# Kernel optimization log

Hardware: AMD Instinct MI355X
Metric: run time of the kernel (lower is better)

Reference implementation:

```python
import jax, jax.numpy as jnp
import numpy as np

B, S, H, M, E = 64, 512, 1024, 26, 676  # batch, seq, hidden, max_nodes, max_edges (M*M)


def setup_inputs() -> dict:
    key = jax.random.key(0)
    ks = jax.random.split(key, 16)
    seq = jax.random.normal(ks[0], (B, S, H), jnp.float32)
    # ragged, strictly-increasing sentence-end offsets in [1, S-1], zero-padded tail
    rng = np.random.RandomState(0)
    off = np.zeros((B, M - 1), np.int64)
    for b in range(B):
        c = rng.randint(5, M)  # count of valid offsets per sample (ragged)
        off[b, :c] = np.sort(rng.choice(np.arange(1, S), size=c, replace=False))
    s = 1.0 / np.sqrt(H)
    s3 = 1.0 / np.sqrt(3 * H)
    return {
        'sequence_outputs': seq,
        'proof_offsets': jnp.asarray(off),
        'node_labels': jax.random.randint(ks[1], (B, M), 0, 2),
        'edge_labels': jax.random.randint(ks[2], (B, E), 0, 2),
        'W_naf': jax.random.normal(ks[3], (H, H), jnp.float32) * s,
        'b_naf': jnp.zeros((H,), jnp.float32),
        'W_cd': jax.random.normal(ks[4], (H, H), jnp.float32) * s,
        'b_cd': jnp.zeros((H,), jnp.float32),
        'W_co': jax.random.normal(ks[5], (H, 2), jnp.float32) * s,
        'b_co': jnp.zeros((2,), jnp.float32),
        'W_nd': jax.random.normal(ks[6], (H, H), jnp.float32) * s,
        'b_nd': jnp.zeros((H,), jnp.float32),
        'W_no': jax.random.normal(ks[7], (H, 2), jnp.float32) * s,
        'b_no': jnp.zeros((2,), jnp.float32),
        'W_ed': jax.random.normal(ks[8], (3 * H, H), jnp.float32) * s3,
        'b_ed': jnp.zeros((H,), jnp.float32),
        'W_eo': jax.random.normal(ks[9], (H, 2), jnp.float32) * s,
        'b_eo': jnp.zeros((2,), jnp.float32),
    }


def reference(sequence_outputs, proof_offsets, node_labels, edge_labels,
              W_naf, b_naf, W_cd, b_cd, W_co, b_co,
              W_nd, b_nd, W_no, b_no, W_ed, b_ed, W_eo, b_eo):
    Bx, Sx, Hx = sequence_outputs.shape
    Mx = node_labels.shape[1]
    Ex = edge_labels.shape[1]

    cls = sequence_outputs[:, 0, :]                       # [B,H]
    naf = cls @ W_naf + b_naf                             # NAF node embedding
    logits = jnp.tanh(cls @ W_cd + b_cd) @ W_co + b_co    # RobertaClassificationHead (eval: dropout=id)

    # segment-mean pooling via inclusive prefix sums: segment j = tokens (prev_j, off_j]
    P = jnp.cumsum(sequence_outputs, axis=1)              # [B,S,H]
    off = proof_offsets                                   # [B,M-1]
    prev = jnp.concatenate([jnp.zeros((Bx, 1), off.dtype), off[:, :-1]], axis=1)
    valid = off > 0                                       # [B,M-1]
    seg_sum = (jnp.take_along_axis(P, off[..., None], axis=1)
               - jnp.take_along_axis(P, prev[..., None], axis=1))  # [B,M-1,H]
    seg_len = jnp.maximum(off - prev, 1).astype(sequence_outputs.dtype)
    seg_mean = seg_sum / seg_len[..., None] * valid[..., None]

    count = valid.sum(axis=1)                             # nodes per sample (excl. NAF)
    # node embeddings: seg means at 0..count-1, NAF at index count, zeros after
    node_full = jnp.concatenate([seg_mean, jnp.zeros((Bx, 1, Hx), seg_mean.dtype)], axis=1)  # [B,M,H]
    idx = jnp.arange(Mx)
    node_full = node_full + (idx[None, :, None] == count[:, None, None]) * naf[:, None, :]

    # all-pairs edge features over n=count+1 nodes, row-major flat k=i*n+j, zero-padded to E
    n = count + 1                                         # [B]
    k = jnp.arange(Ex)                                    # [E]
    i = jnp.clip(k[None, :] // n[:, None], 0, Mx - 1)     # [B,E]
    j = jnp.clip(k[None, :] % n[:, None], 0, Mx - 1)
    valid_e = (k[None, :] < (n * n)[:, None])[..., None]
    ni = jnp.take_along_axis(node_full, i[..., None], axis=1)  # [B,E,H]
    nj = jnp.take_along_axis(node_full, j[..., None], axis=1)
    edge = jnp.concatenate([nj, ni, nj - ni], axis=-1) * valid_e  # [B,E,3H]

    node_logits = jnp.tanh(node_full @ W_nd + b_nd) @ W_no + b_no
    edge_logits = jnp.tanh(edge @ W_ed + b_ed) @ W_eo + b_eo
    return (logits, node_logits, edge_logits)
```

## Files before the change

### kernel.cpp

```cpp
#include <hip/hip_runtime.h>
#include <hip/hip_bf16.h>

#define B_ 64
#define S_ 512
#define H_ 1024
#define M_ 26
#define E_ 676

typedef short bf16x8 __attribute__((ext_vector_type(8)));
typedef float f32x4 __attribute__((ext_vector_type(4)));

__device__ __forceinline__ void gload16(const void* g, void* l) {
    __builtin_amdgcn_global_load_lds((const __attribute__((address_space(1))) unsigned int*)g,
                                     (__attribute__((address_space(3))) unsigned int*)l,
                                     16, 0, 0);
}

__device__ __forceinline__ float tanh_fast(float x) {
    float e = __expf(2.0f * x);
    return 1.0f - 2.0f * __builtin_amdgcn_rcpf(e + 1.0f);
}

__global__ __launch_bounds__(256) void k_stage1(
    const float* __restrict__ seq, const int* __restrict__ off,
    const float* __restrict__ Wnaf, const float* __restrict__ Wcd,
    const float* __restrict__ Wnd, const float* __restrict__ Wed,
    const float* __restrict__ bed, const float* __restrict__ Weo,
    const float* __restrict__ beo,
    __hip_bfloat16* __restrict__ Wt, int* __restrict__ count,
    float* __restrict__ econ, float* __restrict__ naf, float* __restrict__ cdh,
    float* __restrict__ node_sum) {
    __shared__ float smem[2048];
    int bid = blockIdx.x;
    int tid = threadIdx.x;

    if (bid < 1024) {
        int chunk = bid & 15, b = bid >> 4;
        int* offs = (int*)smem;
        int* cs = (int*)smem + 28;
        if (tid < M_ - 1) offs[tid] = off[b * (M_ - 1) + tid];
        __syncthreads();
        if (tid == 0) {
            int c = 0;
            while (c < M_ - 1 && offs[c] > 0) c++;
            cs[0] = c; cs[1] = (c > 0) ? offs[c - 1] : 0;
        }
        __syncthreads();
        int c = cs[0], offmax = cs[1];
        int t0 = chunk * 32;
        int ts = max(t0, 1), te = min(t0 + 31, offmax);
        if (ts > te) return;
        int m = 0;
        while (m < c && offs[m] < ts) m++;
        const float4* sq = (const float4*)(seq + (size_t)b * S_ * H_) + tid;
        int t = ts;
        while (t <= te) {
            int segEnd = min(offs[m], te);
            int L = segEnd - t + 1;
            const float4* p = sq + (size_t)t * (H_ / 4);
            float4 a0 = make_float4(0, 0, 0, 0);
            float4 a1 = a0, a2 = a0, a3 = a0;
            int u = 0;
            for (; u + 4 <= L; u += 4) {
                float4 v0 = p[(size_t)(u + 0) * (H_ / 4)];
                float4 v1 = p[(size_t)(u + 1) * (H_ / 4)];
                float4 v2 = p[(size_t)(u + 2) * (H_ / 4)];
                float4 v3 = p[(size_t)(u + 3) * (H_ / 4)];
                a0.x += v0.x; a0.y += v0.y; a0.z += v0.z; a0.w += v0.w;
                a1.x += v1.x; a1.y += v1.y; a1.z += v1.z; a1.w += v1.w;
                a2.x += v2.x; a2.y += v2.y; a2.z += v2.z; a2.w += v2.w;
                a3.x += v3.x; a3.y += v3.y; a3.z += v3.z; a3.w += v3.w;
            }
            for (; u < L; ++u) {
                float4 v0 = p[(size_t)u * (H_ / 4)];
                a0.x += v0.x; a0.y += v0.y; a0.z += v0.z; a0.w += v0.w;
            }
            a0.x += a1.x + a2.x + a3.x;
            a0.y += a1.y + a2.y + a3.y;
            a0.z += a1.z + a2.z + a3.z;
            a0.w += a1.w + a2.w + a3.w;
            float* dst = node_sum + ((size_t)(b * M_ + m)) * H_ + tid * 4;
            atomicAdd(dst + 0, a0.x); atomicAdd(dst + 1, a0.y);
            atomicAdd(dst + 2, a0.z); atomicAdd(dst + 3, a0.w);
            t = segEnd + 1;
            m++;
        }
    } else if (bid < 4096) {
        float (*T)[33] = (float(*)[33])smem;
        int e = bid - 1024;
        int s = e >> 10, rem = e & 1023;
        int bx = rem & 31, by = rem >> 5;
        int c = tid & 31, r0 = tid >> 5;
        const int HH = H_ * H_;
#pragma unroll
        for (int i = 0; i < 4; ++i) {
            int r = r0 + 8 * i;
            size_t k = by * 32 + r, n = bx * 32 + c;
            float v;
            if (s == 0)      v = Wnd[k * H_ + n];
            else if (s == 1) v = Wed[k * H_ + n] + Wed[2 * HH + k * H_ + n];
            else             v = Wed[HH + k * H_ + n] - Wed[2 * HH + k * H_ + n];
            T[r][c] = v;
        }
        __syncthreads();
#pragma unroll
        for (int i = 0; i < 4; ++i) {
            int rr = r0 + 8 * i;
            Wt[(size_t)(s * H_ + bx * 32 + rr) * H_ + by * 32 + c] = __float2bfloat16(T[c][rr]);
        }
    } else if (bid == 4096) {
        if (tid < 64) {
            int b = tid;
            int c = 0;
            for (int m = 0; m < M_ - 1; ++m) c += (off[b * (M_ - 1) + m] > 0) ? 1 : 0;
            count[b] = c;
        }
    } else if (bid == 4097) {
        float* s0 = smem; float* s1 = smem + 256;
        float a0 = 0.f, a1 = 0.f;
        for (int h = tid; h < H_; h += 256) {
            float t = tanh_fast(bed[h]);
            a0 += t * Weo[h * 2 + 0];
            a1 += t * Weo[h * 2 + 1];
        }
        s0[tid] = a0; s1[tid] = a1; __syncthreads();
        for (int o = 128; o > 0; o >>= 1) {
            if (tid < o) { s0[tid] += s0[tid + o]; s1[tid] += s1[tid + o]; }
            __syncthreads();
        }
        if (tid == 0) { econ[0] = s0[0] + beo[0]; econ[1] = s1[0] + beo[1]; }
    } else {
        float (*As)[64] = (float(*)[64])smem;
        float (*Bs)[64] = (float(*)[64])(smem + 1024);
        int e = bid - 4098;
        int bx = e & 31;
        int kbase = (e >> 5) * 128;
        const float* W;
        float* dst;
        int cbase;
        if (bx < 16) { W = Wnaf; dst = naf; cbase = bx * 64; }
        else         { W = Wcd;  dst = cdh; cbase = (bx - 16) * 64; }
        int tx = tid % 16, ty = tid / 16;
        float c[4][4] = {};
        int la_row = tid / 4;
        int la_k4  = (tid % 4) * 4;
        int lb_k   = tid / 16;
        int lb_c4  = (tid % 16) * 4;
        for (int k0 = 0; k0 < 128; k0 += 16) {
            float4 a = *(const float4*)(seq + (size_t)la_row * S_ * H_ + kbase + k0 + la_k4);
            *(float4*)(&Bs[lb_k][lb_c4]) =
                *(const float4*)(W + (size_t)(kbase + k0 + lb_k) * H_ + cbase + lb_c4);
            As[la_k4 + 0][la_row] = a.x;
            As[la_k4 + 1][la_row] = a.y;
            As[la_k4 + 2][la_row] = a.z;
            As[la_k4 + 3][la_row] = a.w;
            __syncthreads();
#pragma unroll
            for (int kk = 0; kk < 16; ++kk) {
                float4 av = *(const float4*)(&As[kk][ty * 4]);
                float4 bv = *(const float4*)(&Bs[kk][tx * 4]);
                c[0][0] += av.x * bv.x; c[0][1] += av.x * bv.y; c[0][2] += av.x * bv.z; c[0][3] += av.x * bv.w;
                c[1][0] += av.y * bv.x; c[1][1] += av.y * bv.y; c[1][2] += av.y * bv.z; c[1][3] += av.y * bv.w;
                c[2][0] += av.z * bv.x; c[2][1] += av.z * bv.y; c[2][2] += av.z * bv.z; c[2][3] += av.z * bv.w;
                c[3][0] += av.w * bv.x; c[3][1] += av.w * bv.y; c[3][2] += av.w * bv.z; c[3][3] += av.w * bv.w;
            }
            __syncthreads();
        }
#pragma unroll
        for (int i = 0; i < 4; ++i)
#pragma unroll
            for (int j = 0; j < 4; ++j)
                atomicAdd(dst + (size_t)(ty * 4 + i) * H_ + cbase + tx * 4 + j, c[i][j]);
    }
}

__global__ __launch_bounds__(256) void k_stage2(
    const float* __restrict__ sums, const int* __restrict__ off,
    const int* __restrict__ count, const float* __restrict__ naf,
    const float* __restrict__ bnaf, __hip_bfloat16* __restrict__ nodeB,
    const float* __restrict__ cdh, const float* __restrict__ bcd,
    const float* __restrict__ Wco, const float* __restrict__ bco,
    float* __restrict__ out) {
    __shared__ float smem[512];
    int bid = blockIdx.x;
    int tid = threadIdx.x;
    if (bid < 1664) {
        int b = bid / 26, m = bid - b * 26;
        int cnt = count[b];
        float4 v = make_float4(0, 0, 0, 0);
        const float4* row = (const float4*)(sums + ((size_t)(b * M_ + m)) * H_);
        if (m < M_ - 1) {
            int o = off[b * (M_ - 1) + m];
            if (o > 0) {
                int prev = (m > 0) ? off[b * (M_ - 1) + m - 1] : 0;
                float inv = 1.0f / (float)max(o - prev, 1);
                float4 s = row[tid];
                v = make_float4(s.x * inv, s.y * inv, s.z * inv, s.w * inv);
            }
        }
        if (m == cnt) {
            float4 a = ((const float4*)(naf + (size_t)b * H_))[tid];
            float4 bb = ((const float4*)bnaf)[tid];
            v.x += a.x + bb.x; v.y += a.y + bb.y; v.z += a.z + bb.z; v.w += a.w + bb.w;
        }
        __hip_bfloat16 __attribute__((aligned(8))) h[4] = {
            __float2bfloat16(v.x), __float2bfloat16(v.y),
            __float2bfloat16(v.z), __float2bfloat16(v.w)};
        *(ushort4*)(nodeB + ((size_t)(b * M_ + m)) * H_ + tid * 4) = *(const ushort4*)h;
    } else {
        int b = bid - 1664;
        float* s0 = smem; float* s1 = smem + 256;
        float a0 = 0.f, a1 = 0.f;
        for (int h = tid; h < H_; h += 256) {
            float t = tanh_fast(cdh[(size_t)b * H_ + h] + bcd[h]);
            a0 += t * Wco[h * 2 + 0];
            a1 += t * Wco[h * 2 + 1];
        }
        s0[tid] = a0; s1[tid] = a1; __syncthreads();
        for (int o = 128; o > 0; o >>= 1) {
            if (tid < o) { s0[tid] += s0[tid + o]; s1[tid] += s1[tid + o]; }
            __syncthreads();
        }
        if (tid == 0) { out[b * 2 + 0] = s0[0] + bco[0]; out[b * 2 + 1] = s1[0] + bco[1]; }
    }
}

#define GM 1664
#define GN 3072
#define GK 1024
__global__ __launch_bounds__(256) void k_mfma(const __hip_bfloat16* __restrict__ A,
                                              const __hip_bfloat16* __restrict__ Bt,
                                              float* __restrict__ C) {
    __shared__ __hip_bfloat16 As[128 * 32];
    __shared__ __hip_bfloat16 Bs[128 * 32];
    int tid = threadIdx.x;
    int wid = tid >> 6, ln = tid & 63;
    int row0 = blockIdx.y * 128, col0 = blockIdx.x * 128;
    const __hip_bfloat16* ga = A + (size_t)(row0 + wid * 16 + (ln >> 2)) * GK + (ln & 3) * 8;
    const __hip_bfloat16* gb = Bt + (size_t)(col0 + wid * 16 + (ln >> 2)) * GK + (ln & 3) * 8;
    __hip_bfloat16* lA = As + wid * 512;
    __hip_bfloat16* lB = Bs + wid * 512;
    int mrow = (wid >> 1) * 64, ncol = (wid & 1) * 64;
    int l15 = ln & 15, l4 = ln >> 4;
    f32x4 acc[4][4] = {};
    const __hip_bfloat16* pa = As + (size_t)(mrow + l15) * 32 + l4 * 8;
    const __hip_bfloat16* pb = Bs + (size_t)(ncol + l15) * 32 + l4 * 8;
    for (int k0 = 0; k0 < GK; k0 += 32) {
        gload16(ga, lA);
        gload16(ga + 64 * GK, lA + 2048);
        gload16(gb, lB);
        gload16(gb + 64 * GK, lB + 2048);
        ga += 32; gb += 32;
        __syncthreads();
        bf16x8 af[4], bf[4];
#pragma unroll
        for (int mi = 0; mi < 4; ++mi) af[mi] = *(const bf16x8*)(pa + mi * 16 * 32);
#pragma unroll
        for (int ni = 0; ni < 4; ++ni) bf[ni] = *(const bf16x8*)(pb + ni * 16 * 32);
#pragma unroll
        for (int mi = 0; mi < 4; ++mi)
#pragma unroll
            for (int ni = 0; ni < 4; ++ni)
                acc[mi][ni] = __builtin_amdgcn_mfma_f32_16x16x32_bf16(af[mi], bf[ni],
                                                                      acc[mi][ni], 0, 0, 0);
        __syncthreads();
    }
#pragma unroll
    for (int mi = 0; mi < 4; ++mi)
#pragma unroll
        for (int ni = 0; ni < 4; ++ni) {
            f32x4 v = acc[mi][ni];
            size_t r = row0 + mrow + mi * 16 + l4 * 4;
            size_t cc = col0 + ncol + ni * 16 + l15;
            C[(r + 0) * GN + cc] = v[0];
            C[(r + 1) * GN + cc] = v[1];
            C[(r + 2) * GN + cc] = v[2];
            C[(r + 3) * GN + cc] = v[3];
        }
}

__global__ __launch_bounds__(256) void k_stage4(
    const float* __restrict__ Cm, const int* __restrict__ count,
    const float* __restrict__ bnd, const float* __restrict__ Wno,
    const float* __restrict__ bno, const float* __restrict__ bed,
    const float* __restrict__ Weo, const float* __restrict__ beo,
    const float* __restrict__ econ, float* __restrict__ out_n,
    float* __restrict__ out_e) {
    int bid = blockIdx.x;
    int wid = threadIdx.x >> 6, lane = threadIdx.x & 63;
    if (bid < 416) {
        int r = bid * 4 + wid;
        const float4* src = (const float4*)(Cm + (size_t)r * GN);
        float a0 = 0.f, a1 = 0.f;
#pragma unroll
        for (int it = 0; it < 4; ++it) {
            int h = lane * 4 + it * 256;
            float4 s = src[lane + it * 64];
            float4 bb = *(const float4*)(bnd + h);
            float t0 = tanh_fast(s.x + bb.x), t1 = tanh_fast(s.y + bb.y);
            float t2 = tanh_fast(s.z + bb.z), t3 = tanh_fast(s.w + bb.w);
            a0 += t0 * Wno[h * 2 + 0] + t1 * Wno[h * 2 + 2] + t2 * Wno[h * 2 + 4] + t3 * Wno[h * 2 + 6];
            a1 += t0 * Wno[h * 2 + 1] + t1 * Wno[h * 2 + 3] + t2 * Wno[h * 2 + 5] + t3 * Wno[h * 2 + 7];
        }
        for (int o = 32; o > 0; o >>= 1) { a0 += __shfl_down(a0, o); a1 += __shfl_down(a1, o); }
        if (lane == 0) { out_n[(size_t)r * 2 + 0] = a0 + bno[0]; out_n[(size_t)r * 2 + 1] = a1 + bno[1]; }
    } else {
        int e = bid - 416;
        int b = e >> 4;
        int wg = (e & 15) * 4 + wid;
        int n = count[b] + 1;
        int n2 = n * n;
        float4 bed4[4], w04[4], w14[4];
#pragma unroll
        for (int it = 0; it < 4; ++it) {
            int h = lane * 4 + it * 256;
            bed4[it] = *(const float4*)(bed + h);
            w04[it] = make_float4(Weo[h * 2 + 0], Weo[h * 2 + 2], Weo[h * 2 + 4], Weo[h * 2 + 6]);
            w14[it] = make_float4(Weo[h * 2 + 1], Weo[h * 2 + 3], Weo[h * 2 + 5], Weo[h * 2 + 7]);
        }
        float e0 = econ[0], e1 = econ[1];
        float b0 = beo[0], b1 = beo[1];
        for (int k = wg; k < E_; k += 64) {
            float* dst = out_e + ((size_t)b * E_ + k) * 2;
            if (k >= n2) {
                if (lane == 0) { dst[0] = e0; dst[1] = e1; }
                continue;
            }
            int i = k / n, j = k - i * n;
            const float4* U4 = (const float4*)(Cm + (size_t)(b * M_ + j) * GN + H_);
            const float4* V4 = (const float4*)(Cm + (size_t)(b * M_ + i) * GN + 2 * H_);
            float a0 = 0.f, a1 = 0.f;
#pragma unroll
            for (int it = 0; it < 4; ++it) {
                float4 u = U4[lane + it * 64];
                float4 v = V4[lane + it * 64];
                float t0 = tanh_fast(u.x + v.x + bed4[it].x);
                float t1 = tanh_fast(u.y + v.y + bed4[it].y);
                float t2 = tanh_fast(u.z + v.z + bed4[it].z);
                float t3 = tanh_fast(u.w + v.w + bed4[it].w);
                a0 += t0 * w04[it].x + t1 * w04[it].y + t2 * w04[it].z + t3 * w04[it].w;
                a1 += t0 * w14[it].x + t1 * w14[it].y + t2 * w14[it].z + t3 * w14[it].w;
            }
            for (int o = 32; o > 0; o >>= 1) { a0 += __shfl_down(a0, o); a1 += __shfl_down(a1, o); }
            if (lane == 0) { dst[0] = a0 + b0; dst[1] = a1 + b1; }
        }
    }
}

extern "C" void kernel_launch(void* const* d_in, const int* in_sizes, int n_in,
                              void* d_out, int out_size, void* d_ws, size_t ws_size,
                              hipStream_t stream) {
    const float* seq  = (const float*)d_in[0];
    const int*   off  = (const int*)d_in[1];
    const float* Wnaf = (const float*)d_in[4];  const float* bnaf = (const float*)d_in[5];
    const float* Wcd  = (const float*)d_in[6];  const float* bcd  = (const float*)d_in[7];
    const float* Wco  = (const float*)d_in[8];  const float* bco  = (const float*)d_in[9];
    const float* Wnd  = (const float*)d_in[10]; const float* bnd  = (const float*)d_in[11];
    const float* Wno  = (const float*)d_in[12]; const float* bno  = (const float*)d_in[13];
    const float* Wed  = (const float*)d_in[14]; const float* bed  = (const float*)d_in[15];
    const float* Weo  = (const float*)d_in[16]; const float* beo  = (const float*)d_in[17];
    float* out = (float*)d_out;

    float* ws = (float*)d_ws;
    size_t p = 0;
    float* nodeS = ws + p;  p += (size_t)B_ * M_ * H_;
    float* naf   = ws + p;  p += (size_t)B_ * H_;
    float* cdh   = ws + p;  p += (size_t)B_ * H_;
    __hip_bfloat16* nodeB = (__hip_bfloat16*)(ws + p); p += (size_t)B_ * M_ * H_ / 2;
    __hip_bfloat16* Wt    = (__hip_bfloat16*)(ws + p); p += (size_t)3 * H_ * H_ / 2;
    float* Cbuf  = ws + p;  p += (size_t)B_ * M_ * 3 * H_;
    int*   cnt   = (int*)(ws + p); p += 64;
    float* econ  = ws + p;  p += 2;

    hipMemsetAsync(nodeS, 0, ((size_t)B_ * M_ * H_ + 2 * (size_t)B_ * H_) * sizeof(float),
                   stream);

    k_stage1<<<dim3(4354), 256, 0, stream>>>(seq, off, Wnaf, Wcd, Wnd, Wed, bed, Weo, beo,
                                             Wt, cnt, econ, naf, cdh, nodeS);
    k_stage2<<<dim3(1728), 256, 0, stream>>>(nodeS, off, cnt, naf, bnaf, nodeB,
                                             cdh, bcd, Wco, bco, out);
    k_mfma<<<dim3(GN / 128, GM / 128), 256, 0, stream>>>(nodeB, Wt, Cbuf);
    k_stage4<<<dim3(1440), 256, 0, stream>>>(Cbuf, cnt, bnd, Wno, bno, bed, Weo, beo, econ,
                                             out + B_ * 2, out + B_ * 2 + B_ * M_ * 2);
}
```

Measured before the change: 318.4 us.

## Split segment-sum into own kernel and merge Wed transpose reads

Moves the segment-sum pooling out of the fused stage-1 kernel into its own launch and halves the token chunk per block, so twice as many blocks share the ragged sequence reads. The remaining auxiliary work goes into a second kernel. There, the two Wed-derived transposed slices are now built by one block that reads the third Wed slice once instead of twice. The GEMM blocks are also moved to the front of the grid so they start first. The cost is an extra kernel launch and serialization between the two kernels, plus more atomics at chunk boundaries.

```diff
diff --git a/kernel.cpp b/kernel.cpp
--- a/kernel.cpp
+++ b/kernel.cpp
@@ -21,120 +21,79 @@
     return 1.0f - 2.0f * __builtin_amdgcn_rcpf(e + 1.0f);
 }
 
-__global__ __launch_bounds__(256) void k_stage1(
+__global__ __launch_bounds__(256) void k_segk(const float* __restrict__ seq,
+                                              const int* __restrict__ off,
+                                              float* __restrict__ node_sum) {
+    __shared__ int offs[32];
+    __shared__ int cs[2];
+    int bid = blockIdx.x;
+    int tid = threadIdx.x;
+    int chunk = bid & 31, b = bid >> 5;
+    if (tid < M_ - 1) offs[tid] = off[b * (M_ - 1) + tid];
+    __syncthreads();
+    if (tid == 0) {
+        int c = 0;
+        while (c < M_ - 1 && offs[c] > 0) c++;
+        cs[0] = c; cs[1] = (c > 0) ? offs[c - 1] : 0;
+    }
+    __syncthreads();
+    int c = cs[0], offmax = cs[1];
+    int t0 = chunk * 16;
+    int ts = max(t0, 1), te = min(t0 + 15, offmax);
+    if (ts > te) return;
+    int m = 0;
+    while (m < c && offs[m] < ts) m++;
+    const float4* sq = (const float4*)(seq + (size_t)b * S_ * H_) + tid;
+    int t = ts;
+    while (t <= te) {
+        int segEnd = min(offs[m], te);
+        int L = segEnd - t + 1;
+        const float4* p = sq + (size_t)t * (H_ / 4);
+        float4 a0 = make_float4(0, 0, 0, 0);
+        float4 a1 = a0, a2 = a0, a3 = a0;
+        int u = 0;
+        for (; u + 4 <= L; u += 4) {
+            float4 v0 = p[(size_t)(u + 0) * (H_ / 4)];
+            float4 v1 = p[(size_t)(u + 1) * (H_ / 4)];
+            float4 v2 = p[(size_t)(u + 2) * (H_ / 4)];
+            float4 v3 = p[(size_t)(u + 3) * (H_ / 4)];
+            a0.x += v0.x; a0.y += v0.y; a0.z += v0.z; a0.w += v0.w;
+            a1.x += v1.x; a1.y += v1.y; a1.z += v1.z; a1.w += v1.w;
+            a2.x += v2.x; a2.y += v2.y; a2.z += v2.z; a2.w += v2.w;
+            a3.x += v3.x; a3.y += v3.y; a3.z += v3.z; a3.w += v3.w;
+        }
+        for (; u < L; ++u) {
+            float4 v0 = p[(size_t)u * (H_ / 4)];
+            a0.x += v0.x; a0.y += v0.y; a0.z += v0.z; a0.w += v0.w;
+        }
+        a0.x += a1.x + a2.x + a3.x;
+        a0.y += a1.y + a2.y + a3.y;
+        a0.z += a1.z + a2.z + a3.z;
+        a0.w += a1.w + a2.w + a3.w;
+        float* dst = node_sum + ((size_t)(b * M_ + m)) * H_ + tid * 4;
+        atomicAdd(dst + 0, a0.x); atomicAdd(dst + 1, a0.y);
+        atomicAdd(dst + 2, a0.z); atomicAdd(dst + 3, a0.w);
+        t = segEnd + 1;
+        m++;
+    }
+}
+
+__global__ __launch_bounds__(256) void k_aux(
     const float* __restrict__ seq, const int* __restrict__ off,
     const float* __restrict__ Wnaf, const float* __restrict__ Wcd,
     const float* __restrict__ Wnd, const float* __restrict__ Wed,
     const float* __restrict__ bed, const float* __restrict__ Weo,
     const float* __restrict__ beo,
     __hip_bfloat16* __restrict__ Wt, int* __restrict__ count,
-    float* __restrict__ econ, float* __restrict__ naf, float* __restrict__ cdh,
-    float* __restrict__ node_sum) {
-    __shared__ float smem[2048];
+    float* __restrict__ econ, float* __restrict__ naf, float* __restrict__ cdh) {
+    __shared__ float smem[2112];
     int bid = blockIdx.x;
     int tid = threadIdx.x;
-
-    if (bid < 1024) {
-        int chunk = bid & 15, b = bid >> 4;
-        int* offs = (int*)smem;
-        int* cs = (int*)smem + 28;
-        if (tid < M_ - 1) offs[tid] = off[b * (M_ - 1) + tid];
-        __syncthreads();
-        if (tid == 0) {
-            int c = 0;
-            while (c < M_ - 1 && offs[c] > 0) c++;
-            cs[0] = c; cs[1] = (c > 0) ? offs[c - 1] : 0;
-        }
-        __syncthreads();
-        int c = cs[0], offmax = cs[1];
-        int t0 = chunk * 32;
-        int ts = max(t0, 1), te = min(t0 + 31, offmax);
-        if (ts > te) return;
-        int m = 0;
-        while (m < c && offs[m] < ts) m++;
-        const float4* sq = (const float4*)(seq + (size_t)b * S_ * H_) + tid;
-        int t = ts;
-        while (t <= te) {
-            int segEnd = min(offs[m], te);
-            int L = segEnd - t + 1;
-            const float4* p = sq + (size_t)t * (H_ / 4);
-            float4 a0 = make_float4(0, 0, 0, 0);
-            float4 a1 = a0, a2 = a0, a3 = a0;
-            int u = 0;
-            for (; u + 4 <= L; u += 4) {
-                float4 v0 = p[(size_t)(u + 0) * (H_ / 4)];
-                float4 v1 = p[(size_t)(u + 1) * (H_ / 4)];
-                float4 v2 = p[(size_t)(u + 2) * (H_ / 4)];
-                float4 v3 = p[(size_t)(u + 3) * (H_ / 4)];
-                a0.x += v0.x; a0.y += v0.y; a0.z += v0.z; a0.w += v0.w;
-                a1.x += v1.x; a1.y += v1.y; a1.z += v1.z; a1.w += v1.w;
-                a2.x += v2.x; a2.y += v2.y; a2.z += v2.z; a2.w += v2.w;
-                a3.x += v3.x; a3.y += v3.y; a3.z += v3.z; a3.w += v3.w;
-            }
-            for (; u < L; ++u) {
-                float4 v0 = p[(size_t)u * (H_ / 4)];
-                a0.x += v0.x; a0.y += v0.y; a0.z += v0.z; a0.w += v0.w;
-            }
-            a0.x += a1.x + a2.x + a3.x;
-            a0.y += a1.y + a2.y + a3.y;
-            a0.z += a1.z + a2.z + a3.z;
-            a0.w += a1.w + a2.w + a3.w;
-            float* dst = node_sum + ((size_t)(b * M_ + m)) * H_ + tid * 4;
-            atomicAdd(dst + 0, a0.x); atomicAdd(dst + 1, a0.y);
-            atomicAdd(dst + 2, a0.z); atomicAdd(dst + 3, a0.w);
-            t = segEnd + 1;
-            m++;
-        }
-    } else if (bid < 4096) {
-        float (*T)[33] = (float(*)[33])smem;
-        int e = bid - 1024;
-        int s = e >> 10, rem = e & 1023;
-        int bx = rem & 31, by = rem >> 5;
-        int c = tid & 31, r0 = tid >> 5;
-        const int HH = H_ * H_;
-#pragma unroll
-        for (int i = 0; i < 4; ++i) {
-            int r = r0 + 8 * i;
-            size_t k = by * 32 + r, n = bx * 32 + c;
-            float v;
-            if (s == 0)      v = Wnd[k * H_ + n];
-            else if (s == 1) v = Wed[k * H_ + n] + Wed[2 * HH + k * H_ + n];
-            else             v = Wed[HH + k * H_ + n] - Wed[2 * HH + k * H_ + n];
-            T[r][c] = v;
-        }
-        __syncthreads();
-#pragma unroll
-        for (int i = 0; i < 4; ++i) {
-            int rr = r0 + 8 * i;
-            Wt[(size_t)(s * H_ + bx * 32 + rr) * H_ + by * 32 + c] = __float2bfloat16(T[c][rr]);
-        }
-    } else if (bid == 4096) {
-        if (tid < 64) {
-            int b = tid;
-            int c = 0;
-            for (int m = 0; m < M_ - 1; ++m) c += (off[b * (M_ - 1) + m] > 0) ? 1 : 0;
-            count[b] = c;
-        }
-    } else if (bid == 4097) {
-        float* s0 = smem; float* s1 = smem + 256;
-        float a0 = 0.f, a1 = 0.f;
-        for (int h = tid; h < H_; h += 256) {
-            float t = tanh_fast(bed[h]);
-            a0 += t * Weo[h * 2 + 0];
-            a1 += t * Weo[h * 2 + 1];
-        }
-        s0[tid] = a0; s1[tid] = a1; __syncthreads();
-        for (int o = 128; o > 0; o >>= 1) {
-            if (tid < o) { s0[tid] += s0[tid + o]; s1[tid] += s1[tid + o]; }
-            __syncthreads();
-        }
-        if (tid == 0) { econ[0] = s0[0] + beo[0]; econ[1] = s1[0] + beo[1]; }
-    } else {
+    if (bid < 256) {
         float (*As)[64] = (float(*)[64])smem;
         float (*Bs)[64] = (float(*)[64])(smem + 1024);
-        int e = bid - 4098;
-        int bx = e & 31;
-        int kbase = (e >> 5) * 128;
+        int bx = bid & 31;
+        int kbase = (bid >> 5) * 128;
         const float* W;
         float* dst;
         int cbase;
@@ -171,6 +130,68 @@
 #pragma unroll
             for (int j = 0; j < 4; ++j)
                 atomicAdd(dst + (size_t)(ty * 4 + i) * H_ + cbase + tx * 4 + j, c[i][j]);
+    } else if (bid < 1280) {
+        float (*T1)[33] = (float(*)[33])smem;
+        float (*T2)[33] = (float(*)[33])(smem + 1056);
+        int e = bid - 256;
+        int bx = e & 31, by = e >> 5;
+        int cc = tid & 31, r0 = tid >> 5;
+        const int HH = H_ * H_;
+#pragma unroll
+        for (int i = 0; i < 4; ++i) {
+            int r = r0 + 8 * i;
+            size_t k = by * 32 + r, n = bx * 32 + cc;
+            float w1 = Wed[k * H_ + n];
+            float w2 = Wed[HH + k * H_ + n];
+            float w3 = Wed[2 * HH + k * H_ + n];
+            T1[r][cc] = w1 + w3;
+            T2[r][cc] = w2 - w3;
+        }
+        __syncthreads();
+#pragma unroll
+        for (int i = 0; i < 4; ++i) {
+            int rr = r0 + 8 * i;
+            Wt[(size_t)(H_ + bx * 32 + rr) * H_ + by * 32 + cc]     = __float2bfloat16(T1[cc][rr]);
+            Wt[(size_t)(2 * H_ + bx * 32 + rr) * H_ + by * 32 + cc] = __float2bfloat16(T2[cc][rr]);
+        }
+    } else if (bid < 2304) {
+        float (*T)[33] = (float(*)[33])smem;
+        int e = bid - 1280;
+        int bx = e & 31, by = e >> 5;
+        int cc = tid & 31, r0 = tid >> 5;
+#pragma unroll
+        for (int i = 0; i < 4; ++i) {
+            int r = r0 + 8 * i;
+            size_t k = by * 32 + r, n = bx * 32 + cc;
+            T[r][cc] = Wnd[k * H_ + n];
+        }
+        __syncthreads();
+#pragma unroll
+        for (int i = 0; i < 4; ++i) {
+            int rr = r0 + 8 * i;
+            Wt[(size_t)(bx * 32 + rr) * H_ + by * 32 + cc] = __float2bfloat16(T[cc][rr]);
+        }
+    } else if (bid == 2304) {
+        if (tid < 64) {
+            int b = tid;
+            int c = 0;
+            for (int m = 0; m < M_ - 1; ++m) c += (off[b * (M_ - 1) + m] > 0) ? 1 : 0;
+            count[b] = c;
+        }
+    } else {
+        float* s0 = smem; float* s1 = smem + 256;
+        float a0 = 0.f, a1 = 0.f;
+        for (int h = tid; h < H_; h += 256) {
+            float t = tanh_fast(bed[h]);
+            a0 += t * Weo[h * 2 + 0];
+            a1 += t * Weo[h * 2 + 1];
+        }
+        s0[tid] = a0; s1[tid] = a1; __syncthreads();
+        for (int o = 128; o > 0; o >>= 1) {
+            if (tid < o) { s0[tid] += s0[tid + o]; s1[tid] += s1[tid + o]; }
+            __syncthreads();
+        }
+        if (tid == 0) { econ[0] = s0[0] + beo[0]; econ[1] = s1[0] + beo[1]; }
     }
 }
 
@@ -375,8 +396,9 @@
     hipMemsetAsync(nodeS, 0, ((size_t)B_ * M_ * H_ + 2 * (size_t)B_ * H_) * sizeof(float),
                    stream);
 
-    k_stage1<<<dim3(4354), 256, 0, stream>>>(seq, off, Wnaf, Wcd, Wnd, Wed, bed, Weo, beo,
-                                             Wt, cnt, econ, naf, cdh, nodeS);
+    k_segk<<<dim3(2048), 256, 0, stream>>>(seq, off, nodeS);
+    k_aux<<<dim3(2306), 256, 0, stream>>>(seq, off, Wnaf, Wcd, Wnd, Wed, bed, Weo, beo,
+                                          Wt, cnt, econ, naf, cdh);
     k_stage2<<<dim3(1728), 256, 0, stream>>>(nodeS, off, cnt, naf, bnaf, nodeB,
                                              cdh, bcd, Wco, bco, out);
     k_mfma<<<dim3(GN / 128, GM / 128), 256, 0, stream>>>(nodeB, Wt, Cbuf);
```

Result: slower. 333.4 us (+4.7%).
